# Kernel optimization log

Hardware: AMD Instinct MI355X
Metric: run time of the kernel (lower is better)

The kernel has to match this reference:

```python
import jax, jax.numpy as jnp
import numpy as np

B, S, D, H, W, FFN = 2, 4096, 1024, 16, 256, 4096
HD = D // H


def layer_norm(x, g, b):
    mu = x.mean(-1, keepdims=True)
    var = ((x - mu) ** 2).mean(-1, keepdims=True)
    return (x - mu) * jax.lax.rsqrt(var + 1e-5) * g + b


def setup_inputs() -> dict:
    key = jax.random.key(0)
    ks = jax.random.split(key, 16)
    s = 1.0 / np.sqrt(D)
    inp = {
        "x": jax.random.normal(ks[0], (B, S, D), jnp.float32),
        "Wq": jax.random.normal(ks[1], (D, D), jnp.float32) * s,
        "bq": jnp.zeros((D,), jnp.float32),
        "Wk": jax.random.normal(ks[2], (D, D), jnp.float32) * s,
        "bk": jnp.zeros((D,), jnp.float32),
        "Wv": jax.random.normal(ks[3], (D, D), jnp.float32) * s,
        "bv": jnp.zeros((D,), jnp.float32),
        "Wo": jax.random.normal(ks[4], (D, D), jnp.float32) * s,
        "bo": jnp.zeros((D,), jnp.float32),
        "g1": jnp.ones((D,), jnp.float32),
        "b1": jnp.zeros((D,), jnp.float32),
        "W1": jax.random.normal(ks[5], (D, FFN), jnp.float32) * s,
        "c1": jnp.zeros((FFN,), jnp.float32),
        "W2": jax.random.normal(ks[6], (FFN, D), jnp.float32) * (1.0 / np.sqrt(FFN)),
        "c2": jnp.zeros((D,), jnp.float32),
        "g2": jnp.ones((D,), jnp.float32),
        "b2": jnp.zeros((D,), jnp.float32),
    }
    return inp


def sliding_window_attn(x, Wq, bq, Wk, bk, Wv, bv, Wo, bo):
    b, s, d = x.shape
    nb = s // W
    # project and chunk into blocks of size W: (B, nb, W, H, HD)
    q = (x @ Wq + bq).reshape(b, nb, W, H, HD)
    k = (x @ Wk + bk).reshape(b, nb, W, H, HD)
    v = (x @ Wv + bv).reshape(b, nb, W, H, HD)
    pad = [(0, 0), (1, 1), (0, 0), (0, 0), (0, 0)]
    kp, vp = jnp.pad(k, pad), jnp.pad(v, pad)
    # each block attends to [prev, self, next] blocks -> (B, nb, 3W, H, HD)
    kc = jnp.concatenate([kp[:, :-2], kp[:, 1:-1], kp[:, 2:]], axis=2)
    vc = jnp.concatenate([vp[:, :-2], vp[:, 1:-1], vp[:, 2:]], axis=2)
    scale = jnp.asarray(1.0 / np.sqrt(HD), x.dtype)
    scores = jnp.einsum("bnqhd,bnkhd->bhnqk", q, kc) * scale
    i = jnp.arange(W)[:, None]
    j = jnp.arange(3 * W)[None, :]
    band = jnp.abs(i + W - j) <= W  # (W, 3W): |q_pos - k_pos| <= W
    kidx = jnp.arange(nb)[:, None] * W - W + jnp.arange(3 * W)[None, :]
    valid = (kidx >= 0) & (kidx < s)  # (nb, 3W): drop padded halo blocks
    mask = band[None, :, :] & valid[:, None, :]  # (nb, W, 3W)
    scores = jnp.where(mask[None, None], scores, jnp.asarray(-1e9, x.dtype))
    attn = jax.nn.softmax(scores, axis=-1)
    out = jnp.einsum("bhnqk,bnkhd->bnqhd", attn, vc).reshape(b, s, d)
    return out @ Wo + bo


def reference(x, Wq, bq, Wk, bk, Wv, bv, Wo, bo, g1, b1, W1, c1, W2, c2, g2, b2):
    a = sliding_window_attn(x, Wq, bq, Wk, bk, Wv, bv, Wo, bo)
    h = layer_norm(a + x, g1, b1)  # dropout = identity (eval mode)
    f = jax.nn.gelu(h @ W1 + c1) @ W2 + c2
    return layer_norm(f + h, g2, b2)
```

## Files before the change

### kernel.cpp

```cpp
#include <hip/hip_runtime.h>
#include <hip/hip_bf16.h>

#define BB 2
#define SS 4096
#define DD 1024
#define HH 16
#define WW 256
#define FF 4096
#define HDIM 64
#define NBLK (SS / WW)
#define MROWS (BB * SS)

typedef short bfrag8 __attribute__((ext_vector_type(8)));
typedef float floatx4 __attribute__((ext_vector_type(4)));

__device__ __forceinline__ float bf2f(ushort u) {
    union { uint i; float f; } c; c.i = ((uint)u) << 16; return c.f;
}
__device__ __forceinline__ ushort f2bf(float f) {
    union { float f; uint i; } c; c.f = f;
    uint r = (c.i + 0x7FFFu + ((c.i >> 16) & 1u)) >> 16;
    return (ushort)r;
}
__device__ __forceinline__ float gelu_fast(float x) {
    float z2 = 1.5957691216057308f * x * (1.f + 0.044715f * x * x);
    return x / (1.f + __expf(-z2));
}

__device__ __forceinline__ void gload_lds16(const ushort* g, ushort* l) {
    __builtin_amdgcn_global_load_lds(
        (const __attribute__((address_space(1))) void*)g,
        (__attribute__((address_space(3))) void*)l, 16, 0, 0);
}

__global__ __launch_bounds__(256) void cvt_f32_bf16(
    const float* __restrict__ in, ushort* __restrict__ out)
{
    size_t i = ((size_t)blockIdx.x * 256 + threadIdx.x) * 4;
    float4 v = *(const float4*)(in + i);
    union { ushort u[4]; uint2 d; } t;
    t.u[0] = f2bf(v.x); t.u[1] = f2bf(v.y);
    t.u[2] = f2bf(v.z); t.u[3] = f2bf(v.w);
    *(uint2*)(out + i) = t.d;
}

__global__ __launch_bounds__(256) void cvt_transpose_all(
    const float* __restrict__ Wq, const float* __restrict__ Wk,
    const float* __restrict__ Wv, const float* __restrict__ Wo,
    const float* __restrict__ W1, const float* __restrict__ W2,
    ushort* __restrict__ WqkvT, ushort* __restrict__ WoT,
    ushort* __restrict__ W1t, ushort* __restrict__ W2t)
{
    __shared__ ushort sT[32][33];
    const int z = blockIdx.z;
    const float* in; ushort* out; int K, N, n0, k0;
    if (z < 4) {
        if (blockIdx.x >= 32) return;
        in  = (z == 0) ? Wq : (z == 1) ? Wk : (z == 2) ? Wv : Wo;
        out = (z < 3) ? WqkvT + (size_t)z * 1024 * 1024 : WoT;
        K = 1024; N = 1024;
        n0 = blockIdx.x * 32; k0 = blockIdx.y * 32;
    } else if (z == 4) {
        in = W1; out = W1t; K = 1024; N = 4096;
        n0 = blockIdx.x * 32; k0 = blockIdx.y * 32;
    } else {
        in = W2; out = W2t; K = 4096; N = 1024;
        n0 = blockIdx.y * 32; k0 = blockIdx.x * 32;
    }

    const int r  = threadIdx.x >> 3;
    const int c4 = (threadIdx.x & 7) * 4;

    float4 v = *(const float4*)(in + (size_t)(k0 + r) * N + n0 + c4);
    sT[c4 + 0][r] = f2bf(v.x);
    sT[c4 + 1][r] = f2bf(v.y);
    sT[c4 + 2][r] = f2bf(v.z);
    sT[c4 + 3][r] = f2bf(v.w);
    __syncthreads();
    union { ushort u[4]; uint2 d; } t;
#pragma unroll
    for (int e = 0; e < 4; ++e) t.u[e] = sT[r][c4 + e];
    *(uint2*)(out + (size_t)(n0 + r) * K + k0 + c4) = t.d;
}

__global__ __launch_bounds__(256) void gemm_bt(
    const ushort* __restrict__ A, const ushort* __restrict__ Bt,
    const float* __restrict__ bias, ushort* __restrict__ C,
    int M, int N, int K, int act)
{
    __shared__ ushort sA[128 * 64];
    __shared__ ushort sB[128 * 64];

    const int tid  = threadIdx.x;
    const int nx   = N >> 7;
    const int nyg  = (M >> 7) >> 3;
    const int gid  = blockIdx.x;
    const int j    = gid >> 3;
    const int m0   = ((gid & 7) * nyg + j / nx) * 128;
    const int n0   = (j % nx) * 128;
    const int wave = tid >> 6;
    const int lane = tid & 63;
    const int wm   = (wave >> 1) * 64;
    const int wn   = (wave & 1) * 64;
    const int lrow = lane & 15;
    const int quad = lane >> 4;

    floatx4 acc[4][4];
#pragma unroll
    for (int i = 0; i < 4; ++i)
#pragma unroll
        for (int j2 = 0; j2 < 4; ++j2)
            acc[i][j2] = (floatx4){0.f, 0.f, 0.f, 0.f};

    for (int k0 = 0; k0 < K; k0 += 64) {
#pragma unroll
        for (int it = 0; it < 4; ++it) {
            int c    = it * 256 + tid;
            int row  = c >> 3;
            int scol = ((c ^ (row & 7)) & 7) << 3;
            gload_lds16(A  + (size_t)(m0 + row) * K + k0 + scol, &sA[c * 8]);
            gload_lds16(Bt + (size_t)(n0 + row) * K + k0 + scol, &sB[c * 8]);
        }
        __syncthreads();

#pragma unroll
        for (int ks = 0; ks < 2; ++ks) {
            bfrag8 af[4], bfv[4];
#pragma unroll
            for (int mt = 0; mt < 4; ++mt) {
                int row = wm + mt * 16 + lrow;
                int G   = ks * 4 + quad;
                af[mt] = *(const bfrag8*)&sA[row * 64 + (((G ^ row) & 7) << 3) + ((G >> 3) << 6)];
            }
#pragma unroll
            for (int nt = 0; nt < 4; ++nt) {
                int row = wn + nt * 16 + lrow;
                int G   = ks * 4 + quad;
                bfv[nt] = *(const bfrag8*)&sB[row * 64 + (((G ^ row) & 7) << 3) + ((G >> 3) << 6)];
            }
#pragma unroll
            for (int mt = 0; mt < 4; ++mt)
#pragma unroll
                for (int nt = 0; nt < 4; ++nt)
                    acc[mt][nt] = __builtin_amdgcn_mfma_f32_16x16x32_bf16(
                        bfv[nt], af[mt], acc[mt][nt], 0, 0, 0);
        }
        __syncthreads();
    }

#pragma unroll
    for (int nt = 0; nt < 4; ++nt) {
        int nb = n0 + wn + nt * 16 + quad * 4;
        union { float4 v; float f[4]; } b4;
        b4.v = *(const float4*)(bias + nb);
#pragma unroll
        for (int mt = 0; mt < 4; ++mt) {
            int row = m0 + wm + mt * 16 + lrow;
            union { ushort u[4]; uint2 d; } t;
#pragma unroll
            for (int r = 0; r < 4; ++r) {
                float v = acc[mt][nt][r] + b4.f[r];
                if (act) v = gelu_fast(v);
                t.u[r] = f2bf(v);
            }
            *(uint2*)(C + (size_t)row * N + nb) = t.d;
        }
    }
}

__global__ __launch_bounds__(256) void gemm_qkv(
    const ushort* __restrict__ A, const ushort* __restrict__ Bt,
    const float* __restrict__ bq, const float* __restrict__ bk,
    const float* __restrict__ bv,
    ushort* __restrict__ qb, ushort* __restrict__ kb, ushort* __restrict__ vT)
{
    __shared__ ushort sA[128 * 64];
    __shared__ ushort sB[128 * 64];
    const int K = DD;

    const int tid  = threadIdx.x;
    const int nx   = 24, nyg = 8;
    const int gid  = blockIdx.x;
    const int j    = gid >> 3;
    const int m0   = ((gid & 7) * nyg + j / nx) * 128;
    const int n0   = (j % nx) * 128;
    const int wave = tid >> 6;
    const int lane = tid & 63;
    const int wm   = (wave >> 1) * 64;
    const int wn   = (wave & 1) * 64;
    const int lrow = lane & 15;
    const int quad = lane >> 4;
    const int sel  = n0 >> 10;

    floatx4 acc[4][4];
#pragma unroll
    for (int i = 0; i < 4; ++i)
#pragma unroll
        for (int j2 = 0; j2 < 4; ++j2)
            acc[i][j2] = (floatx4){0.f, 0.f, 0.f, 0.f};

    for (int k0 = 0; k0 < K; k0 += 64) {
#pragma unroll
        for (int it = 0; it < 4; ++it) {
            int c    = it * 256 + tid;
            int row  = c >> 3;
            int scol = ((c ^ (row & 7)) & 7) << 3;
            gload_lds16(A  + (size_t)(m0 + row) * K + k0 + scol, &sA[c * 8]);
            gload_lds16(Bt + (size_t)(n0 + row) * K + k0 + scol, &sB[c * 8]);
        }
        __syncthreads();

#pragma unroll
        for (int ks = 0; ks < 2; ++ks) {
            bfrag8 af[4], bfv[4];
#pragma unroll
            for (int mt = 0; mt < 4; ++mt) {
                int row = wm + mt * 16 + lrow;
                int G   = ks * 4 + quad;
                af[mt] = *(const bfrag8*)&sA[row * 64 + (((G ^ row) & 7) << 3)];
            }
#pragma unroll
            for (int nt = 0; nt < 4; ++nt) {
                int row = wn + nt * 16 + lrow;
                int G   = ks * 4 + quad;
                bfv[nt] = *(const bfrag8*)&sB[row * 64 + (((G ^ row) & 7) << 3)];
            }
            if (sel < 2) {
#pragma unroll
                for (int mt = 0; mt < 4; ++mt)
#pragma unroll
                    for (int nt = 0; nt < 4; ++nt)
                        acc[mt][nt] = __builtin_amdgcn_mfma_f32_16x16x32_bf16(
                            bfv[nt], af[mt], acc[mt][nt], 0, 0, 0);
            } else {
#pragma unroll
                for (int mt = 0; mt < 4; ++mt)
#pragma unroll
                    for (int nt = 0; nt < 4; ++nt)
                        acc[mt][nt] = __builtin_amdgcn_mfma_f32_16x16x32_bf16(
                            af[mt], bfv[nt], acc[mt][nt], 0, 0, 0);
            }
        }
        __syncthreads();
    }

    if (sel < 2) {
        ushort* C = (sel == 0) ? qb : kb;
        const float* bias = (sel == 0) ? bq : bk;
        const int colbase = n0 + wn;
#pragma unroll
        for (int nt = 0; nt < 4; ++nt) {
            int nb = (colbase + nt * 16 + quad * 4) & 1023;
            union { float4 v; float f[4]; } b4;
            b4.v = *(const float4*)(bias + nb);
#pragma unroll
            for (int mt = 0; mt < 4; ++mt) {
                int row = m0 + wm + mt * 16 + lrow;
                union { ushort u[4]; uint2 d; } t;
#pragma unroll
                for (int r = 0; r < 4; ++r) t.u[r] = f2bf(acc[mt][nt][r] + b4.f[r]);
                *(uint2*)(C + (size_t)row * DD + nb) = t.d;
            }
        }
    } else {
        const int colbase = n0 + wn;
#pragma unroll
        for (int nt = 0; nt < 4; ++nt) {
            int cc = (colbase + nt * 16 + lrow) & 1023;
            int h = cc >> 6, dh = cc & 63;
            float bb = bv[cc];
#pragma unroll
            for (int mt = 0; mt < 4; ++mt) {
                int row0 = m0 + wm + mt * 16 + (quad << 2);
                int b = row0 >> 12, s = row0 & 4095;
                union { ushort u[4]; uint2 d; } t;
#pragma unroll
                for (int r = 0; r < 4; ++r) t.u[r] = f2bf(acc[mt][nt][r] + bb);
                *(uint2*)(vT + (size_t)(((b * HH + h) * HDIM + dh)) * SS + s) = t.d;
            }
        }
    }
}

__global__ __launch_bounds__(64, 2) void attn_flash(
    const ushort* __restrict__ q, const ushort* __restrict__ k,
    const ushort* __restrict__ vT, ushort* __restrict__ out)
{
    __shared__ ushort sP[64 * 72];

    const int qt = blockIdx.x, h = blockIdx.y, b = blockIdx.z;
    const int lane = threadIdx.x;
    const int c16  = lane & 15;
    const int quad = lane >> 4;
    const float CC = 0.18033688011112042f;

    bfrag8 qf[4][2];
    {
        const size_t qbase = ((size_t)b * SS + qt * 64) * DD + h * HDIM;
#pragma unroll
        for (int nt = 0; nt < 4; ++nt)
#pragma unroll
            for (int ks = 0; ks < 2; ++ks)
                qf[nt][ks] = *(const bfrag8*)(q + qbase +
                    (size_t)(nt * 16 + c16) * DD + ks * 32 + quad * 8);
    }

    floatx4 oacc[4][4];
#pragma unroll
    for (int i = 0; i < 4; ++i)
#pragma unroll
        for (int j = 0; j < 4; ++j)
            oacc[i][j] = (floatx4){0.f, 0.f, 0.f, 0.f};
    float mrow[4], lsum[4];
#pragma unroll
    for (int i = 0; i < 4; ++i) { mrow[i] = -1e30f; lsum[i] = 0.f; }

    const int st0 = (qt - 4 > 0) ? qt - 4 : 0;
    const int st1 = (qt + 4 < 63) ? qt + 4 : 63;
    const size_t kb_b  = (size_t)b * SS * DD + h * HDIM;
    const size_t vT_b  = (size_t)((b * HH + h) * HDIM) * SS;

    for (int st = st0; st <= st1; ++st) {
        const int dlt = st - qt;

        floatx4 sacc[4][4];
#pragma unroll
        for (int i = 0; i < 4; ++i)
#pragma unroll
            for (int j = 0; j < 4; ++j)
                sacc[i][j] = (floatx4){0.f, 0.f, 0.f, 0.f};
#pragma unroll
        for (int ks = 0; ks < 2; ++ks) {
            bfrag8 kf[4];
#pragma unroll
            for (int mt = 0; mt < 4; ++mt)
                kf[mt] = *(const bfrag8*)(k + kb_b +
                    (size_t)(st * 64 + mt * 16 + c16) * DD + ks * 32 + quad * 8);
#pragma unroll
            for (int mt = 0; mt < 4; ++mt)
#pragma unroll
                for (int nt = 0; nt < 4; ++nt)
                    sacc[mt][nt] = __builtin_amdgcn_mfma_f32_16x16x32_bf16(
                        kf[mt], qf[nt][ks], sacc[mt][nt], 0, 0, 0);
        }

        if (dlt == 4 || dlt == -4) {
#pragma unroll
            for (int mt = 0; mt < 4; ++mt)
#pragma unroll
                for (int nt = 0; nt < 4; ++nt)
#pragma unroll
                    for (int r = 0; r < 4; ++r) {
                        int kl = mt * 16 + quad * 4 + r;
                        int ql = nt * 16 + c16;
                        bool ok = (dlt < 0) ? (kl >= ql) : (kl <= ql);
                        if (!ok) sacc[mt][nt][r] = -1e30f;
                    }
        }

        float pm[4];
#pragma unroll
        for (int nt = 0; nt < 4; ++nt) {
            float a0 = fmaxf(fmaxf(sacc[0][nt][0], sacc[0][nt][1]),
                             fmaxf(sacc[0][nt][2], sacc[0][nt][3]));
            float a1 = fmaxf(fmaxf(sacc[1][nt][0], sacc[1][nt][1]),
                             fmaxf(sacc[1][nt][2], sacc[1][nt][3]));
            float a2 = fmaxf(fmaxf(sacc[2][nt][0], sacc[2][nt][1]),
                             fmaxf(sacc[2][nt][2], sacc[2][nt][3]));
            float a3 = fmaxf(fmaxf(sacc[3][nt][0], sacc[3][nt][1]),
                             fmaxf(sacc[3][nt][2], sacc[3][nt][3]));
            pm[nt] = fmaxf(fmaxf(a0, a1), fmaxf(a2, a3));
            pm[nt] = fmaxf(pm[nt], __shfl_xor(pm[nt], 16, 64));
            pm[nt] = fmaxf(pm[nt], __shfl_xor(pm[nt], 32, 64));
        }
        float al[4];
#pragma unroll
        for (int nt = 0; nt < 4; ++nt) {
            float mn = fmaxf(mrow[nt], pm[nt]);
            al[nt] = exp2f((mrow[nt] - mn) * CC);
            mrow[nt] = mn;
        }
        float ps[4] = {0.f, 0.f, 0.f, 0.f};
#pragma unroll
        for (int mt = 0; mt < 4; ++mt)
#pragma unroll
            for (int nt = 0; nt < 4; ++nt)
#pragma unroll
                for (int r = 0; r < 4; ++r) {
                    float p = exp2f((sacc[mt][nt][r] - mrow[nt]) * CC);
                    sacc[mt][nt][r] = p;
                    ps[nt] += p;
                }
#pragma unroll
        for (int nt = 0; nt < 4; ++nt) {
            ps[nt] += __shfl_xor(ps[nt], 16, 64);
            ps[nt] += __shfl_xor(ps[nt], 32, 64);
            lsum[nt] = lsum[nt] * al[nt] + ps[nt];
        }

#pragma unroll
        for (int mt = 0; mt < 4; ++mt)
#pragma unroll
            for (int nt = 0; nt < 4; ++nt) {
                int row = nt * 16 + c16;
                int g   = (2 * mt + (quad >> 1)) ^ (row & 3);
                union { ushort u[4]; uint2 d; } t;
#pragma unroll
                for (int r = 0; r < 4; ++r) t.u[r] = f2bf(sacc[mt][nt][r]);
                *(uint2*)&sP[row * 72 + g * 8 + (quad & 1) * 4] = t.d;
            }

#pragma unroll
        for (int dt = 0; dt < 4; ++dt)
#pragma unroll
            for (int nq = 0; nq < 4; ++nq)
#pragma unroll
                for (int r = 0; r < 4; ++r)
                    oacc[dt][nq][r] *= al[nq];

#pragma unroll
        for (int ks = 0; ks < 2; ++ks) {
            bfrag8 vf[4], pf[4];
#pragma unroll
            for (int dt = 0; dt < 4; ++dt)
                vf[dt] = *(const bfrag8*)(vT + vT_b +
                    (size_t)(dt * 16 + c16) * SS + st * 64 + ks * 32 + quad * 8);
#pragma unroll
            for (int nq = 0; nq < 4; ++nq) {
                int row = nq * 16 + c16;
                int g   = (4 * ks + quad) ^ (row & 3);
                pf[nq] = *(const bfrag8*)&sP[row * 72 + g * 8];
            }
#pragma unroll
            for (int dt = 0; dt < 4; ++dt)
#pragma unroll
                for (int nq = 0; nq < 4; ++nq)
                    oacc[dt][nq] = __builtin_amdgcn_mfma_f32_16x16x32_bf16(
                        vf[dt], pf[nq], oacc[dt][nq], 0, 0, 0);
        }
    }

#pragma unroll
    for (int nq = 0; nq < 4; ++nq) {
        float inv = 1.f / lsum[nq];
        size_t rbase = ((size_t)b * SS + qt * 64 + nq * 16 + c16) * DD + h * HDIM;
#pragma unroll
        for (int dt = 0; dt < 4; ++dt) {
            union { ushort u[4]; uint2 d; } t;
#pragma unroll
            for (int r = 0; r < 4; ++r) t.u[r] = f2bf(oacc[dt][nq][r] * inv);
            *(uint2*)(out + rbase + dt * 16 + quad * 4) = t.d;
        }
    }
}

__device__ __forceinline__ void ldv4(const float* p, float* o) {
    float4 v = *(const float4*)p;
    o[0] = v.x; o[1] = v.y; o[2] = v.z; o[3] = v.w;
}
__device__ __forceinline__ void ldv4(const ushort* p, float* o) {
    union { ushort u[4]; uint2 d; } t;
    t.d = *(const uint2*)p;
#pragma unroll
    for (int e = 0; e < 4; ++e) o[e] = bf2f(t.u[e]);
}
__device__ __forceinline__ void stv4(float* p, const float* v) {
    float4 t; t.x = v[0]; t.y = v[1]; t.z = v[2]; t.w = v[3];
    *(float4*)p = t;
}
__device__ __forceinline__ void stv4(ushort* p, const float* v) {
    union { ushort u[4]; uint2 d; } t;
#pragma unroll
    for (int e = 0; e < 4; ++e) t.u[e] = f2bf(v[e]);
    *(uint2*)p = t.d;
}

template <typename RT, typename OT>
__global__ __launch_bounds__(256) void add_ln(
    const ushort* __restrict__ a, const RT* __restrict__ res,
    const float* __restrict__ g, const float* __restrict__ bb,
    OT* __restrict__ out)
{
    const int row = blockIdx.x;
    const int tid = threadIdx.x;
    const size_t base = (size_t)row * DD + tid * 4;

    float av[4], rv[4], x[4];
    ldv4(a + base, av);
    ldv4(res + base, rv);
    float s1 = 0.f, s2 = 0.f;
#pragma unroll
    for (int e = 0; e < 4; ++e) {
        x[e] = av[e] + rv[e];
        s1 += x[e];
        s2 += x[e] * x[e];
    }
#pragma unroll
    for (int off = 32; off > 0; off >>= 1) {
        s1 += __shfl_down(s1, off, 64);
        s2 += __shfl_down(s2, off, 64);
    }
    __shared__ float r1[4], r2[4];
    const int wave = tid >> 6, lane = tid & 63;
    if (lane == 0) { r1[wave] = s1; r2[wave] = s2; }
    __syncthreads();
    float t1 = r1[0] + r1[1] + r1[2] + r1[3];
    float t2 = r2[0] + r2[1] + r2[2] + r2[3];
    float mu  = t1 * (1.f / DD);
    float var = t2 * (1.f / DD) - mu * mu;
    float rs  = rsqrtf(var + 1e-5f);

    float gv[4], bv[4], y[4];
    ldv4(g + (size_t)tid * 4, gv);
    ldv4(bb + (size_t)tid * 4, bv);
#pragma unroll
    for (int e = 0; e < 4; ++e)
        y[e] = (x[e] - mu) * rs * gv[e] + bv[e];
    stv4(out + base, y);
}

extern "C" void kernel_launch(void* const* d_in, const int* in_sizes, int n_in,
                              void* d_out, int out_size, void* d_ws, size_t ws_size,
                              hipStream_t stream)
{
    (void)in_sizes; (void)n_in; (void)out_size; (void)ws_size;

    const float* x  = (const float*)d_in[0];
    const float* Wq = (const float*)d_in[1];
    const float* bq = (const float*)d_in[2];
    const float* Wk = (const float*)d_in[3];
    const float* bk = (const float*)d_in[4];
    const float* Wv = (const float*)d_in[5];
    const float* bv = (const float*)d_in[6];
    const float* Wo = (const float*)d_in[7];
    const float* bo = (const float*)d_in[8];
    const float* g1 = (const float*)d_in[9];
    const float* b1 = (const float*)d_in[10];
    const float* W1 = (const float*)d_in[11];
    const float* c1 = (const float*)d_in[12];
    const float* W2 = (const float*)d_in[13];
    const float* c2 = (const float*)d_in[14];
    const float* g2 = (const float*)d_in[15];
    const float* b2 = (const float*)d_in[16];
    float* outp = (float*)d_out;

    char* ws = (char*)d_ws;
    const size_t MB = 1024 * 1024;
    ushort* WqkvT = (ushort*)(ws);
    ushort* WoT = (ushort*)(ws + 6  * MB);
    ushort* W1t = (ushort*)(ws + 8  * MB);
    ushort* W2t = (ushort*)(ws + 16 * MB);
    ushort* xb  = (ushort*)(ws + 24 * MB);
    ushort* qb  = (ushort*)(ws + 40 * MB);
    ushort* kb  = (ushort*)(ws + 56 * MB);
    ushort* vT  = (ushort*)(ws + 72 * MB);
    ushort* att = (ushort*)(ws + 88 * MB);
    ushort* aproj = qb;
    ushort* hbuf  = att;
    ushort* m1  = (ushort*)(ws + 24 * MB);
    ushort* fbuf = (ushort*)(ws + 104 * MB);

    dim3 blk(256, 1, 1);
    dim3 gD1((DD / 128) * (MROWS / 128), 1, 1);
    dim3 gQKV1((3 * DD / 128) * (MROWS / 128), 1, 1);
    dim3 gF1((FF / 128) * (MROWS / 128), 1, 1);
    dim3 ga(SS / 64, HH, BB);
    dim3 gl(MROWS, 1, 1);

    hipLaunchKernelGGL(cvt_transpose_all, dim3(128, 32, 6), blk, 0, stream,
                       Wq, Wk, Wv, Wo, W1, W2, WqkvT, WoT, W1t, W2t);
    hipLaunchKernelGGL(cvt_f32_bf16, dim3(8192), blk, 0, stream, x, xb);

    hipLaunchKernelGGL(gemm_qkv, gQKV1, blk, 0, stream, xb, WqkvT, bq, bk, bv, qb, kb, vT);

    hipLaunchKernelGGL(attn_flash, ga, dim3(64, 1, 1), 0, stream, qb, kb, vT, att);

    hipLaunchKernelGGL(gemm_bt, gD1, blk, 0, stream, att, WoT, bo, aproj, MROWS, DD, DD, 0);
    hipLaunchKernelGGL((add_ln<float, ushort>), gl, blk, 0, stream, aproj, x, g1, b1, hbuf);

    hipLaunchKernelGGL(gemm_bt, gF1, blk, 0, stream, hbuf, W1t, c1, m1, MROWS, FF, DD, 1);
    hipLaunchKernelGGL(gemm_bt, gD1, blk, 0, stream, m1, W2t, c2, fbuf, MROWS, DD, FF, 0);
    hipLaunchKernelGGL((add_ln<ushort, float>), gl, blk, 0, stream, fbuf, hbuf, g2, b2, outp);
}
```

Baseline: 504.3 us.

## Replace gemm_bt with 512-thread double-buffered ping-pong GEMM using larger tiles

```diff
diff --git a/kernel.cpp b/kernel.cpp
--- a/kernel.cpp
+++ b/kernel.cpp
@@ -32,6 +32,10 @@
         (const __attribute__((address_space(1))) void*)g,
         (__attribute__((address_space(3))) void*)l, 16, 0, 0);
 }
+
+#define BARRIER() __builtin_amdgcn_s_barrier()
+#define LGKM0() do { asm volatile("s_waitcnt lgkmcnt(0)" ::: "memory"); \
+                     __builtin_amdgcn_sched_barrier(0); } while (0)
 
 __global__ __launch_bounds__(256) void cvt_f32_bf16(
     const float* __restrict__ in, ushort* __restrict__ out)
@@ -83,78 +87,174 @@
     *(uint2*)(out + (size_t)(n0 + r) * K + k0 + c4) = t.d;
 }
 
-__global__ __launch_bounds__(256) void gemm_bt(
+#define RD_A(BUF, MHALF)                                                    \
+    _Pragma("unroll") for (int i_ = 0; i_ < MH; ++i_) {                     \
+        int row_ = wm + ((MHALF) * MH + i_) * 16 + lrow;                    \
+        _Pragma("unroll") for (int ks_ = 0; ks_ < 2; ++ks_) {               \
+            int G_ = ks_ * 4 + quad;                                        \
+            af[i_][ks_] = *(const bfrag8*)&sA[BUF][row_ * 64 +              \
+                                    (((G_ ^ row_) & 7) << 3)];              \
+        }                                                                   \
+    }
+
+#define RD_B(BUF, NHALF)                                                    \
+    _Pragma("unroll") for (int j_ = 0; j_ < NH; ++j_) {                     \
+        int row_ = wn + ((NHALF) * NH + j_) * 16 + lrow;                    \
+        _Pragma("unroll") for (int ks_ = 0; ks_ < 2; ++ks_) {               \
+            int G_ = ks_ * 4 + quad;                                        \
+            bf[(NHALF) * NH + j_][ks_] = *(const bfrag8*)&sB[BUF][row_ * 64 \
+                                    + (((G_ ^ row_) & 7) << 3)];            \
+        }                                                                   \
+    }
+
+#define MFMA_QUAD(MHALF, NHALF)                                             \
+    _Pragma("unroll") for (int i_ = 0; i_ < MH; ++i_)                       \
+    _Pragma("unroll") for (int j_ = 0; j_ < NH; ++j_)                       \
+    _Pragma("unroll") for (int ks_ = 0; ks_ < 2; ++ks_)                     \
+        acc[(MHALF) * MH + i_][(NHALF) * NH + j_] =                         \
+            __builtin_amdgcn_mfma_f32_16x16x32_bf16(                        \
+                bf[(NHALF) * NH + j_][ks_], af[i_][ks_],                    \
+                acc[(MHALF) * MH + i_][(NHALF) * NH + j_], 0, 0, 0);
+
+template <int BM, int BN>
+__global__ __launch_bounds__(512, 2) void gemm8p(
     const ushort* __restrict__ A, const ushort* __restrict__ Bt,
     const float* __restrict__ bias, ushort* __restrict__ C,
     int M, int N, int K, int act)
 {
-    __shared__ ushort sA[128 * 64];
-    __shared__ ushort sB[128 * 64];
-
-    const int tid  = threadIdx.x;
-    const int nx   = N >> 7;
-    const int nyg  = (M >> 7) >> 3;
-    const int gid  = blockIdx.x;
-    const int j    = gid >> 3;
-    const int m0   = ((gid & 7) * nyg + j / nx) * 128;
-    const int n0   = (j % nx) * 128;
+    constexpr int MR = BM / 32;
+    constexpr int NR = BN / 64;
+    constexpr int MH = MR / 2;
+    constexpr int NH = NR / 2;
+    constexpr int ALOADS = BM / 64;
+    constexpr int BLOADS = BN / 64;
+
+    __shared__ ushort sA[2][BM * 64];
+    __shared__ ushort sB[2][BN * 64];
+
+    const int tid = threadIdx.x;
+
+    const int ntn = N / BN;
+    const int ntm = M / BM;
+    const int xcd = blockIdx.x & 7;
+    const int idx = blockIdx.x >> 3;
+    int mi, ni;
+    if (ntn >= 8) {
+        const int nb = ntn >> 3;
+        ni = xcd * nb + (idx % nb);
+        mi = idx / nb;
+    } else {
+        ni = idx % ntn;
+        mi = xcd * (ntm >> 3) + idx / ntn;
+    }
+    const int m0 = mi * BM, n0 = ni * BN;
+
     const int wave = tid >> 6;
     const int lane = tid & 63;
-    const int wm   = (wave >> 1) * 64;
-    const int wn   = (wave & 1) * 64;
+    const int wm   = (wave >> 2) * (BM / 2);
+    const int wn   = (wave & 3) * (BN / 4);
     const int lrow = lane & 15;
     const int quad = lane >> 4;
 
-    floatx4 acc[4][4];
-#pragma unroll
-    for (int i = 0; i < 4; ++i)
-#pragma unroll
-        for (int j2 = 0; j2 < 4; ++j2)
-            acc[i][j2] = (floatx4){0.f, 0.f, 0.f, 0.f};
-
-    for (int k0 = 0; k0 < K; k0 += 64) {
-#pragma unroll
-        for (int it = 0; it < 4; ++it) {
-            int c    = it * 256 + tid;
-            int row  = c >> 3;
-            int scol = ((c ^ (row & 7)) & 7) << 3;
-            gload_lds16(A  + (size_t)(m0 + row) * K + k0 + scol, &sA[c * 8]);
-            gload_lds16(Bt + (size_t)(n0 + row) * K + k0 + scol, &sB[c * 8]);
-        }
-        __syncthreads();
-
-#pragma unroll
-        for (int ks = 0; ks < 2; ++ks) {
-            bfrag8 af[4], bfv[4];
-#pragma unroll
-            for (int mt = 0; mt < 4; ++mt) {
-                int row = wm + mt * 16 + lrow;
-                int G   = ks * 4 + quad;
-                af[mt] = *(const bfrag8*)&sA[row * 64 + (((G ^ row) & 7) << 3) + ((G >> 3) << 6)];
-            }
-#pragma unroll
-            for (int nt = 0; nt < 4; ++nt) {
-                int row = wn + nt * 16 + lrow;
-                int G   = ks * 4 + quad;
-                bfv[nt] = *(const bfrag8*)&sB[row * 64 + (((G ^ row) & 7) << 3) + ((G >> 3) << 6)];
-            }
-#pragma unroll
-            for (int mt = 0; mt < 4; ++mt)
-#pragma unroll
-                for (int nt = 0; nt < 4; ++nt)
-                    acc[mt][nt] = __builtin_amdgcn_mfma_f32_16x16x32_bf16(
-                        bfv[nt], af[mt], acc[mt][nt], 0, 0, 0);
-        }
-        __syncthreads();
-    }
-
-#pragma unroll
-    for (int nt = 0; nt < 4; ++nt) {
+    floatx4 acc[MR][NR];
+#pragma unroll
+    for (int i = 0; i < MR; ++i)
+#pragma unroll
+        for (int j = 0; j < NR; ++j)
+            acc[i][j] = (floatx4){0.f, 0.f, 0.f, 0.f};
+
+    const ushort* aptr[ALOADS];
+    const ushort* bptr[BLOADS];
+#pragma unroll
+    for (int it = 0; it < ALOADS; ++it) {
+        int c = it * 512 + tid;
+        int row = c >> 3;
+        int scol = ((c ^ (row & 7)) & 7) << 3;
+        aptr[it] = A + (size_t)(m0 + row) * K + scol;
+    }
+#pragma unroll
+    for (int it = 0; it < BLOADS; ++it) {
+        int c = it * 512 + tid;
+        int row = c >> 3;
+        int scol = ((c ^ (row & 7)) & 7) << 3;
+        bptr[it] = Bt + (size_t)(n0 + row) * K + scol;
+    }
+
+    auto stage = [&](int buf, int kofs) {
+#pragma unroll
+        for (int it = 0; it < ALOADS; ++it)
+            gload_lds16(aptr[it] + kofs, (ushort*)&sA[buf][(it * 512 + tid) * 8]);
+#pragma unroll
+        for (int it = 0; it < BLOADS; ++it)
+            gload_lds16(bptr[it] + kofs, (ushort*)&sB[buf][(it * 512 + tid) * 8]);
+    };
+
+    const int NT = K >> 6;
+
+    stage(0, 0);
+    stage(1, 64);
+    if constexpr (ALOADS + BLOADS == 8)
+        asm volatile("s_waitcnt vmcnt(8)" ::: "memory");
+    else
+        asm volatile("s_waitcnt vmcnt(6)" ::: "memory");
+    BARRIER();
+
+    bfrag8 af[MH][2];
+    bfrag8 bf[NR][2];
+
+    for (int t = 0; t < NT; ++t) {
+        const int cur = t & 1;
+
+        RD_A(cur, 0)
+        RD_B(cur, 0)
+        BARRIER();
+        LGKM0();
+        __builtin_amdgcn_s_setprio(1);
+        MFMA_QUAD(0, 0)
+        __builtin_amdgcn_s_setprio(0);
+        BARRIER();
+
+        RD_B(cur, 1)
+        BARRIER();
+        LGKM0();
+        __builtin_amdgcn_s_setprio(1);
+        MFMA_QUAD(0, 1)
+        __builtin_amdgcn_s_setprio(0);
+        BARRIER();
+
+        RD_A(cur, 1)
+        BARRIER();
+        LGKM0();
+        __builtin_amdgcn_s_setprio(1);
+        MFMA_QUAD(1, 1)
+        __builtin_amdgcn_s_setprio(0);
+        BARRIER();
+
+        if (t + 2 < NT) stage(cur, (t + 2) * 64);
+        BARRIER();
+        __builtin_amdgcn_s_setprio(1);
+        MFMA_QUAD(1, 0)
+        __builtin_amdgcn_s_setprio(0);
+        if (t + 1 < NT) {
+            if (t + 2 < NT) {
+                if constexpr (ALOADS + BLOADS == 8)
+                    asm volatile("s_waitcnt vmcnt(8)" ::: "memory");
+                else
+                    asm volatile("s_waitcnt vmcnt(6)" ::: "memory");
+            } else {
+                asm volatile("s_waitcnt vmcnt(0)" ::: "memory");
+            }
+        }
+        BARRIER();
+    }
+
+#pragma unroll
+    for (int nt = 0; nt < NR; ++nt) {
         int nb = n0 + wn + nt * 16 + quad * 4;
         union { float4 v; float f[4]; } b4;
         b4.v = *(const float4*)(bias + nb);
 #pragma unroll
-        for (int mt = 0; mt < 4; ++mt) {
+        for (int mt = 0; mt < MR; ++mt) {
             int row = m0 + wm + mt * 16 + lrow;
             union { ushort u[4]; uint2 d; } t;
 #pragma unroll
@@ -561,9 +661,8 @@
     ushort* fbuf = (ushort*)(ws + 104 * MB);
 
     dim3 blk(256, 1, 1);
-    dim3 gD1((DD / 128) * (MROWS / 128), 1, 1);
+    dim3 blk512(512, 1, 1);
     dim3 gQKV1((3 * DD / 128) * (MROWS / 128), 1, 1);
-    dim3 gF1((FF / 128) * (MROWS / 128), 1, 1);
     dim3 ga(SS / 64, HH, BB);
     dim3 gl(MROWS, 1, 1);
 
@@ -575,10 +674,13 @@
 
     hipLaunchKernelGGL(attn_flash, ga, dim3(64, 1, 1), 0, stream, qb, kb, vT, att);
 
-    hipLaunchKernelGGL(gemm_bt, gD1, blk, 0, stream, att, WoT, bo, aproj, MROWS, DD, DD, 0);
+    hipLaunchKernelGGL((gemm8p<128, 256>), dim3(256), blk512, 0, stream,
+                       att, WoT, bo, aproj, MROWS, DD, DD, 0);
     hipLaunchKernelGGL((add_ln<float, ushort>), gl, blk, 0, stream, aproj, x, g1, b1, hbuf);
 
-    hipLaunchKernelGGL(gemm_bt, gF1, blk, 0, stream, hbuf, W1t, c1, m1, MROWS, FF, DD, 1);
-    hipLaunchKernelGGL(gemm_bt, gD1, blk, 0, stream, m1, W2t, c2, fbuf, MROWS, DD, FF, 0);
+    hipLaunchKernelGGL((gemm8p<256, 256>), dim3(512), blk512, 0, stream,
+                       hbuf, W1t, c1, m1, MROWS, FF, DD, 1);
+    hipLaunchKernelGGL((gemm8p<128, 256>), dim3(256), blk512, 0, stream,
+                       m1, W2t, c2, fbuf, MROWS, DD, FF, 0);
     hipLaunchKernelGGL((add_ln<ushort, float>), gl, blk, 0, stream, fbuf, hbuf, g2, b2, outp);
 }
```

Measured after the change: 522.6 us. +3.6%, slower.

## Replace generic GEMM with triple-buffered 128x256 tile kernel using 512 threads

Applied to the files above, without the earlier changes.

```diff
diff --git a/kernel.cpp b/kernel.cpp
--- a/kernel.cpp
+++ b/kernel.cpp
@@ -83,70 +83,139 @@
     *(uint2*)(out + (size_t)(n0 + r) * K + k0 + c4) = t.d;
 }
 
-__global__ __launch_bounds__(256) void gemm_bt(
+__device__ __forceinline__ void gemm_core_128x256(
+    const ushort* __restrict__ A, const ushort* __restrict__ Bt,
+    int K, int m0, int n0, floatx4 (&acc)[4][4])
+{
+    __shared__ __align__(16) ushort sA[3][128 * 64];
+    __shared__ __align__(16) ushort sB[3][256 * 64];
+
+    const int tid  = threadIdx.x;
+    const int lane = tid & 63;
+    const int wave = tid >> 6;
+    const int wm   = (wave >> 2) * 64;
+    const int wn   = (wave & 3) * 64;
+    const int lrow = lane & 15;
+    const int quad = lane >> 4;
+
+#pragma unroll
+    for (int i = 0; i < 4; ++i)
+#pragma unroll
+        for (int j = 0; j < 4; ++j)
+            acc[i][j] = (floatx4){0.f, 0.f, 0.f, 0.f};
+
+    const ushort* aptr[2];
+    const ushort* bptr[4];
+#pragma unroll
+    for (int it = 0; it < 2; ++it) {
+        int c = it * 512 + tid;
+        int row = c >> 3;
+        int scol = ((c ^ (row & 7)) & 7) << 3;
+        aptr[it] = A + (size_t)(m0 + row) * K + scol;
+    }
+#pragma unroll
+    for (int it = 0; it < 4; ++it) {
+        int c = it * 512 + tid;
+        int row = c >> 3;
+        int scol = ((c ^ (row & 7)) & 7) << 3;
+        bptr[it] = Bt + (size_t)(n0 + row) * K + scol;
+    }
+
+    auto stage = [&](int buf, int kofs) {
+#pragma unroll
+        for (int it = 0; it < 2; ++it)
+            gload_lds16(aptr[it] + kofs, (ushort*)&sA[buf][(it * 512 + tid) * 8]);
+#pragma unroll
+        for (int it = 0; it < 4; ++it)
+            gload_lds16(bptr[it] + kofs, (ushort*)&sB[buf][(it * 512 + tid) * 8]);
+    };
+
+    const int NT = K >> 6;
+
+    stage(0, 0);
+    stage(1, 64);
+
+    for (int t = 0; t < NT; ++t) {
+        const int cur = t % 3;
+
+        if (t < NT - 1)
+            asm volatile("s_waitcnt vmcnt(6) lgkmcnt(0)" ::: "memory");
+        else
+            asm volatile("s_waitcnt vmcnt(0) lgkmcnt(0)" ::: "memory");
+        __builtin_amdgcn_s_barrier();
+        __builtin_amdgcn_sched_barrier(0);
+
+        if (t + 2 < NT) stage((t + 2) % 3, (t + 2) * 64);
+
+        bfrag8 af[4][2], bf[4][2];
+#pragma unroll
+        for (int mt = 0; mt < 4; ++mt) {
+            int row = wm + mt * 16 + lrow;
+#pragma unroll
+            for (int ks = 0; ks < 2; ++ks) {
+                int G = ks * 4 + quad;
+                af[mt][ks] = *(const bfrag8*)&sA[cur][row * 64 + (((G ^ row) & 7) << 3)];
+            }
+        }
+#pragma unroll
+        for (int nt = 0; nt < 4; ++nt) {
+            int row = wn + nt * 16 + lrow;
+#pragma unroll
+            for (int ks = 0; ks < 2; ++ks) {
+                int G = ks * 4 + quad;
+                bf[nt][ks] = *(const bfrag8*)&sB[cur][row * 64 + (((G ^ row) & 7) << 3)];
+            }
+        }
+
+        __builtin_amdgcn_s_setprio(1);
+#pragma unroll
+        for (int ks = 0; ks < 2; ++ks)
+#pragma unroll
+            for (int mt = 0; mt < 4; ++mt)
+#pragma unroll
+                for (int nt = 0; nt < 4; ++nt)
+                    acc[mt][nt] = __builtin_amdgcn_mfma_f32_16x16x32_bf16(
+                        bf[nt][ks], af[mt][ks], acc[mt][nt], 0, 0, 0);
+        __builtin_amdgcn_s_setprio(0);
+    }
+}
+
+__device__ __forceinline__ void tile_map(int M, int N, int& m0, int& n0)
+{
+    const int ntn = N >> 8;
+    const int ntm = M >> 7;
+    const int xcd = blockIdx.x & 7;
+    const int idx = blockIdx.x >> 3;
+    int mi, ni;
+    if ((ntn & 7) == 0) {
+        const int nb = ntn >> 3;
+        ni = xcd * nb + idx % nb;
+        mi = idx / nb;
+    } else {
+        ni = idx % ntn;
+        mi = xcd * (ntm >> 3) + idx / ntn;
+    }
+    m0 = mi * 128; n0 = ni * 256;
+}
+
+__global__ __launch_bounds__(512, 1) void gemm_pl(
     const ushort* __restrict__ A, const ushort* __restrict__ Bt,
     const float* __restrict__ bias, ushort* __restrict__ C,
     int M, int N, int K, int act)
 {
-    __shared__ ushort sA[128 * 64];
-    __shared__ ushort sB[128 * 64];
+    int m0, n0;
+    tile_map(M, N, m0, n0);
+
+    floatx4 acc[4][4];
+    gemm_core_128x256(A, Bt, K, m0, n0, acc);
 
     const int tid  = threadIdx.x;
-    const int nx   = N >> 7;
-    const int nyg  = (M >> 7) >> 3;
-    const int gid  = blockIdx.x;
-    const int j    = gid >> 3;
-    const int m0   = ((gid & 7) * nyg + j / nx) * 128;
-    const int n0   = (j % nx) * 128;
+    const int lane = tid & 63;
     const int wave = tid >> 6;
-    const int lane = tid & 63;
-    const int wm   = (wave >> 1) * 64;
-    const int wn   = (wave & 1) * 64;
+    const int wm   = (wave >> 2) * 64;
+    const int wn   = (wave & 3) * 64;
     const int lrow = lane & 15;
     const int quad = lane >> 4;
-
-    floatx4 acc[4][4];
-#pragma unroll
-    for (int i = 0; i < 4; ++i)
-#pragma unroll
-        for (int j2 = 0; j2 < 4; ++j2)
-            acc[i][j2] = (floatx4){0.f, 0.f, 0.f, 0.f};
-
-    for (int k0 = 0; k0 < K; k0 += 64) {
-#pragma unroll
-        for (int it = 0; it < 4; ++it) {
-            int c    = it * 256 + tid;
-            int row  = c >> 3;
-            int scol = ((c ^ (row & 7)) & 7) << 3;
-            gload_lds16(A  + (size_t)(m0 + row) * K + k0 + scol, &sA[c * 8]);
-            gload_lds16(Bt + (size_t)(n0 + row) * K + k0 + scol, &sB[c * 8]);
-        }
-        __syncthreads();
-
-#pragma unroll
-        for (int ks = 0; ks < 2; ++ks) {
-            bfrag8 af[4], bfv[4];
-#pragma unroll
-            for (int mt = 0; mt < 4; ++mt) {
-                int row = wm + mt * 16 + lrow;
-                int G   = ks * 4 + quad;
-                af[mt] = *(const bfrag8*)&sA[row * 64 + (((G ^ row) & 7) << 3) + ((G >> 3) << 6)];
-            }
-#pragma unroll
-            for (int nt = 0; nt < 4; ++nt) {
-                int row = wn + nt * 16 + lrow;
-                int G   = ks * 4 + quad;
-                bfv[nt] = *(const bfrag8*)&sB[row * 64 + (((G ^ row) & 7) << 3) + ((G >> 3) << 6)];
-            }
-#pragma unroll
-            for (int mt = 0; mt < 4; ++mt)
-#pragma unroll
-                for (int nt = 0; nt < 4; ++nt)
-                    acc[mt][nt] = __builtin_amdgcn_mfma_f32_16x16x32_bf16(
-                        bfv[nt], af[mt], acc[mt][nt], 0, 0, 0);
-        }
-        __syncthreads();
-    }
 
 #pragma unroll
     for (int nt = 0; nt < 4; ++nt) {
@@ -561,9 +630,8 @@
     ushort* fbuf = (ushort*)(ws + 104 * MB);
 
     dim3 blk(256, 1, 1);
-    dim3 gD1((DD / 128) * (MROWS / 128), 1, 1);
+    dim3 blk512(512, 1, 1);
     dim3 gQKV1((3 * DD / 128) * (MROWS / 128), 1, 1);
-    dim3 gF1((FF / 128) * (MROWS / 128), 1, 1);
     dim3 ga(SS / 64, HH, BB);
     dim3 gl(MROWS, 1, 1);
 
@@ -575,10 +643,13 @@
 
     hipLaunchKernelGGL(attn_flash, ga, dim3(64, 1, 1), 0, stream, qb, kb, vT, att);
 
-    hipLaunchKernelGGL(gemm_bt, gD1, blk, 0, stream, att, WoT, bo, aproj, MROWS, DD, DD, 0);
+    hipLaunchKernelGGL(gemm_pl, dim3(256), blk512, 0, stream,
+                       att, WoT, bo, aproj, MROWS, DD, DD, 0);
     hipLaunchKernelGGL((add_ln<float, ushort>), gl, blk, 0, stream, aproj, x, g1, b1, hbuf);
 
-    hipLaunchKernelGGL(gemm_bt, gF1, blk, 0, stream, hbuf, W1t, c1, m1, MROWS, FF, DD, 1);
-    hipLaunchKernelGGL(gemm_bt, gD1, blk, 0, stream, m1, W2t, c2, fbuf, MROWS, DD, FF, 0);
+    hipLaunchKernelGGL(gemm_pl, dim3(1024), blk512, 0, stream,
+                       hbuf, W1t, c1, m1, MROWS, FF, DD, 1);
+    hipLaunchKernelGGL(gemm_pl, dim3(256), blk512, 0, stream,
+                       m1, W2t, c2, fbuf, MROWS, DD, FF, 0);
     hipLaunchKernelGGL((add_ln<ushort, float>), gl, blk, 0, stream, fbuf, hbuf, g2, b2, outp);
 }
```

After: 540.1 us. 7.1% more time.

## Add 256x256-tile 8-phase pipelined GEMM for the FFN up-projection

Applied to the files above, without the earlier changes.

```diff
diff --git a/kernel.cpp b/kernel.cpp
--- a/kernel.cpp
+++ b/kernel.cpp
@@ -32,6 +32,11 @@
         (const __attribute__((address_space(1))) void*)g,
         (__attribute__((address_space(3))) void*)l, 16, 0, 0);
 }
+
+#define BAR() __builtin_amdgcn_s_barrier()
+#define SCHED0() __builtin_amdgcn_sched_barrier(0)
+#define LGKM0() do { asm volatile("s_waitcnt lgkmcnt(0)" ::: "memory"); \
+                     __builtin_amdgcn_sched_barrier(0); } while (0)
 
 __global__ __launch_bounds__(256) void cvt_f32_bf16(
     const float* __restrict__ in, ushort* __restrict__ out)
@@ -83,6 +88,173 @@
     *(uint2*)(out + (size_t)(n0 + r) * K + k0 + c4) = t.d;
 }
 
+__global__ __launch_bounds__(512, 1) void gemm_8ph(
+    const ushort* __restrict__ A, const ushort* __restrict__ Bt,
+    const float* __restrict__ bias, ushort* __restrict__ C,
+    int M, int N, int K, int act)
+{
+    __shared__ __align__(16) ushort sA[2][256 * 64];
+    __shared__ __align__(16) ushort sB[2][256 * 64];
+
+    const int tid  = threadIdx.x;
+    const int lane = tid & 63;
+    const int wave = tid >> 6;
+    const int wm   = (wave >> 2) * 128;
+    const int wn   = (wave & 3) * 64;
+    const int lrow = lane & 15;
+    const int quad = lane >> 4;
+
+    const int ntn = N >> 8;
+    const int ntm = M >> 8;
+    const int xcd = blockIdx.x & 7;
+    const int idx = blockIdx.x >> 3;
+    int mi, ni;
+    if ((ntn & 7) == 0) { const int nb = ntn >> 3; ni = xcd * nb + idx % nb; mi = idx / nb; }
+    else                { ni = idx % ntn; mi = xcd * (ntm >> 3) + idx / ntn; }
+    const int m0 = mi * 256, n0 = ni * 256;
+
+    floatx4 acc[8][4];
+#pragma unroll
+    for (int i = 0; i < 8; ++i)
+#pragma unroll
+        for (int j = 0; j < 4; ++j)
+            acc[i][j] = (floatx4){0.f, 0.f, 0.f, 0.f};
+
+    const int scol = ((tid ^ (tid >> 3)) & 7) << 3;
+    const int arow0 = tid >> 3;
+    const int brow0 = ((tid >> 8) << 6) + ((tid >> 3) & 31);
+
+    auto stageA = [&](int buf, int u, int kofs) {
+#pragma unroll
+        for (int it = 0; it < 2; ++it) {
+            int gr = it * 128 + u * 64 + arow0;
+            gload_lds16(A + (size_t)(m0 + gr) * K + kofs + scol,
+                        (ushort*)&sA[buf][gr * 64 + (tid & 7) * 8]);
+        }
+    };
+    auto stageB = [&](int buf, int v, int kofs) {
+#pragma unroll
+        for (int it = 0; it < 2; ++it) {
+            int gr = it * 128 + v * 32 + brow0;
+            gload_lds16(Bt + (size_t)(n0 + gr) * K + kofs + scol,
+                        (ushort*)&sB[buf][gr * 64 + (tid & 7) * 8]);
+        }
+    };
+
+    bfrag8 af[4][2];
+    bfrag8 bf[4][2];
+
+    auto readA = [&](int buf, int h) {
+#pragma unroll
+        for (int mf = 0; mf < 4; ++mf) {
+            int row = wm + (h * 4 + mf) * 16 + lrow;
+#pragma unroll
+            for (int ks = 0; ks < 2; ++ks) {
+                int G = ks * 4 + quad;
+                af[mf][ks] = *(const bfrag8*)&sA[buf][row * 64 + (((G ^ row) & 7) << 3)];
+            }
+        }
+    };
+    auto readB = [&](int buf, int h) {
+#pragma unroll
+        for (int nf = 0; nf < 2; ++nf) {
+            int row = wn + (h * 2 + nf) * 16 + lrow;
+#pragma unroll
+            for (int ks = 0; ks < 2; ++ks) {
+                int G = ks * 4 + quad;
+                bf[h * 2 + nf][ks] = *(const bfrag8*)&sB[buf][row * 64 + (((G ^ row) & 7) << 3)];
+            }
+        }
+    };
+    auto mfma_quad = [&](int mh, int nh) {
+        __builtin_amdgcn_s_setprio(1);
+#pragma unroll
+        for (int mf = 0; mf < 4; ++mf)
+#pragma unroll
+            for (int nf = 0; nf < 2; ++nf)
+#pragma unroll
+                for (int ks = 0; ks < 2; ++ks)
+                    acc[mh * 4 + mf][nh * 2 + nf] =
+                        __builtin_amdgcn_mfma_f32_16x16x32_bf16(
+                            bf[nh * 2 + nf][ks], af[mf][ks],
+                            acc[mh * 4 + mf][nh * 2 + nf], 0, 0, 0);
+        __builtin_amdgcn_s_setprio(0);
+    };
+
+    const int NT = K >> 6;
+
+    stageA(0, 0, 0); stageB(0, 0, 0); stageB(0, 1, 0); stageA(0, 1, 0);
+    stageA(1, 0, 64); stageB(1, 0, 64); stageB(1, 1, 64);
+
+    for (int i = 0; ; ++i) {
+        const int t0 = 2 * i;
+        const bool more = (t0 + 2 < NT);
+        const int kof1 = (t0 + 1) * 64, kof2 = (t0 + 2) * 64, kof3 = (t0 + 3) * 64;
+
+        asm volatile("s_waitcnt vmcnt(6)" ::: "memory");
+        BAR(); SCHED0();
+        readA(0, 0); readB(0, 0);
+        stageA(1, 1, kof1);
+        BAR(); LGKM0();
+        mfma_quad(0, 0);
+        BAR(); SCHED0();
+        readB(0, 1);
+        if (more) stageA(0, 0, kof2);
+        BAR(); LGKM0();
+        mfma_quad(0, 1);
+        BAR(); SCHED0();
+        readA(0, 1);
+        if (more) stageB(0, 0, kof2);
+        BAR(); LGKM0();
+        mfma_quad(1, 1);
+        BAR(); SCHED0();
+        if (more) stageB(0, 1, kof2);
+        BAR();
+        mfma_quad(1, 0);
+        if (more) asm volatile("s_waitcnt vmcnt(6)" ::: "memory");
+        else      asm volatile("s_waitcnt vmcnt(0)" ::: "memory");
+        BAR(); SCHED0();
+        readA(1, 0); readB(1, 0);
+        if (more) stageA(0, 1, kof2);
+        BAR(); LGKM0();
+        mfma_quad(0, 0);
+        BAR(); SCHED0();
+        readB(1, 1);
+        if (more) stageA(1, 0, kof3);
+        BAR(); LGKM0();
+        mfma_quad(0, 1);
+        BAR(); SCHED0();
+        readA(1, 1);
+        if (more) stageB(1, 0, kof3);
+        BAR(); LGKM0();
+        mfma_quad(1, 1);
+        BAR(); SCHED0();
+        if (more) stageB(1, 1, kof3);
+        BAR();
+        mfma_quad(1, 0);
+        if (!more) break;
+    }
+
+#pragma unroll
+    for (int nt = 0; nt < 4; ++nt) {
+        int nb = n0 + wn + nt * 16 + quad * 4;
+        union { float4 v; float f[4]; } b4;
+        b4.v = *(const float4*)(bias + nb);
+#pragma unroll
+        for (int mt = 0; mt < 8; ++mt) {
+            int row = m0 + wm + mt * 16 + lrow;
+            union { ushort u[4]; uint2 d; } t;
+#pragma unroll
+            for (int r = 0; r < 4; ++r) {
+                float v = acc[mt][nt][r] + b4.f[r];
+                if (act) v = gelu_fast(v);
+                t.u[r] = f2bf(v);
+            }
+            *(uint2*)(C + (size_t)row * N + nb) = t.d;
+        }
+    }
+}
+
 __global__ __launch_bounds__(256) void gemm_bt(
     const ushort* __restrict__ A, const ushort* __restrict__ Bt,
     const float* __restrict__ bias, ushort* __restrict__ C,
@@ -561,9 +733,9 @@
     ushort* fbuf = (ushort*)(ws + 104 * MB);
 
     dim3 blk(256, 1, 1);
+    dim3 blk512(512, 1, 1);
     dim3 gD1((DD / 128) * (MROWS / 128), 1, 1);
     dim3 gQKV1((3 * DD / 128) * (MROWS / 128), 1, 1);
-    dim3 gF1((FF / 128) * (MROWS / 128), 1, 1);
     dim3 ga(SS / 64, HH, BB);
     dim3 gl(MROWS, 1, 1);
 
@@ -578,7 +750,8 @@
     hipLaunchKernelGGL(gemm_bt, gD1, blk, 0, stream, att, WoT, bo, aproj, MROWS, DD, DD, 0);
     hipLaunchKernelGGL((add_ln<float, ushort>), gl, blk, 0, stream, aproj, x, g1, b1, hbuf);
 
-    hipLaunchKernelGGL(gemm_bt, gF1, blk, 0, stream, hbuf, W1t, c1, m1, MROWS, FF, DD, 1);
+    hipLaunchKernelGGL(gemm_8ph, dim3(512), blk512, 0, stream,
+                       hbuf, W1t, c1, m1, MROWS, FF, DD, 1);
     hipLaunchKernelGGL(gemm_bt, gD1, blk, 0, stream, m1, W2t, c2, fbuf, MROWS, DD, FF, 0);
     hipLaunchKernelGGL((add_ln<ushort, float>), gl, blk, 0, stream, fbuf, hbuf, g2, b2, outp);
 }
```

New measurement: 536.0 us. 6.3% more time.
